# Kernel tuning notes

Hardware: AMD Instinct MI355X
Metric: run time of the kernel (lower is better)

Reference implementation:

```python
import jax, jax.numpy as jnp
import numpy as np

B, T, D, H = 8, 2048, 2048, 128  # batch, seq_len, d_model, head_size
NEG = -1e9


def setup_inputs() -> dict:
    key = jax.random.key(0)
    k0, k1, k2, k3 = jax.random.split(key, 4)
    x = jax.random.normal(k0, (B, T, D), dtype=jnp.float32)
    s = 1.0 / np.sqrt(D)
    Wq = jax.random.normal(k1, (D, H), dtype=jnp.float32) * s
    Wk = jax.random.normal(k2, (D, H), dtype=jnp.float32) * s
    Wv = jax.random.normal(k3, (D, H), dtype=jnp.float32) * s
    return {"x": x, "Wq": Wq, "Wk": Wk, "Wv": Wv}


def reference(x, Wq, Wk, Wv):
    # projections: [B,T,H]
    q = jnp.einsum('btd,dh->bth', x, Wq)
    k = jnp.einsum('btd,dh->bth', x, Wk)
    v = jnp.einsum('btd,dh->bth', x, Wv)
    # NOTE: module multiplies by sqrt(head_size) (faithful to source)
    wei = jnp.einsum('bqh,bkh->bqk', q, k) * jnp.sqrt(jnp.float32(H))
    causal = jnp.tril(jnp.ones((T, T), dtype=bool))
    wei = jnp.where(causal, wei, jnp.float32(NEG))
    wei = jax.nn.softmax(wei, axis=-1)
    # dropout is identity (deterministic=True / rate=0)
    out = jnp.einsum('bqk,bkh->bqh', wei, v)
    return out
```

## Files before the change

kernel.cpp:

```cpp
#include <hip/hip_runtime.h>
#include <math.h>

#define B_ 8
#define T_ 2048
#define D_ 2048
#define H_ 128
#define M_ (B_ * T_)

typedef __bf16 bf16x8 __attribute__((ext_vector_type(8)));
typedef __bf16 bf16x4 __attribute__((ext_vector_type(4)));
typedef float f32x4 __attribute__((ext_vector_type(4)));

#define MFMA(a, b, c) __builtin_amdgcn_mfma_f32_16x16x32_bf16(a, b, c, 0, 0, 0)

#define QH_OFF 0
#define QL_OFF (1 * 2097152)
#define KH_OFF (2 * 2097152)
#define KL_OFF (3 * 2097152)
#define VT_OFF (4 * 2097152)
#define WTH_OFF (5 * 2097152)
#define WTL_OFF (WTH_OFF + 786432)

__global__ __launch_bounds__(256) void prep_kernel(
    const float* __restrict__ Wq, const float* __restrict__ Wk,
    const float* __restrict__ Wv, __bf16* __restrict__ wt_hi,
    __bf16* __restrict__ wt_lo) {
  const int z = blockIdx.y;
  const int k0 = blockIdx.x * 64;
  const float* W = z == 0 ? Wq : z == 1 ? Wk : Wv;
  __shared__ float tile[64][132];
  const int t = threadIdx.x;
#pragma unroll
  for (int it = 0; it < 8; ++it) {
    int f4 = it * 256 + t;
    int row = f4 >> 5, c = (f4 & 31) << 2;
    *(float4*)&tile[row][c] = *(const float4*)&W[(size_t)(k0 + row) * H_ + c];
  }
  __syncthreads();
  int n = t >> 1, kh = (t & 1) << 5;
  __bf16 h[32], l[32];
#pragma unroll
  for (int kk = 0; kk < 32; ++kk) {
    float x = tile[kh + kk][n];
    __bf16 hi = (__bf16)x;
    h[kk] = hi;
    l[kk] = (__bf16)(x - (float)hi);
  }
  size_t base = (size_t)(z * H_ + n) * D_ + k0 + kh;
#pragma unroll
  for (int c = 0; c < 4; ++c) {
    *(bf16x8*)&wt_hi[base + c * 8] = *(bf16x8*)&h[c * 8];
    *(bf16x8*)&wt_lo[base + c * 8] = *(bf16x8*)&l[c * 8];
  }
}

#define WSTR 36
#define XSTR 72

__global__ __launch_bounds__(512, 2) void proj_kernel(
    const float* __restrict__ X, const __bf16* __restrict__ wt_hi,
    const __bf16* __restrict__ wt_lo, __bf16* __restrict__ qh,
    __bf16* __restrict__ ql, __bf16* __restrict__ kh,
    __bf16* __restrict__ kl, __bf16* __restrict__ vt) {
  __shared__ __align__(16) __bf16 Wh[384 * WSTR];
  __shared__ __align__(16) __bf16 Wl[384 * WSTR];
  __shared__ __align__(16) __bf16 Xs[64 * XSTR];
  const int t = threadIdx.x;
  const int wv = t >> 6, lane = t & 63;
  const int l15 = lane & 15, quad = lane >> 4, q8 = quad * 8;
  const int m0 = blockIdx.x * 64;
  const int nb = wv * 48;
  const int xm = t >> 3, xk = (t & 7) << 2;
  const float* xgp = X + (size_t)(m0 + xm) * D_ + xk;
  f32x4 acc[4][3] = {};
  float4 xr = *(const float4*)xgp;
  bf16x8 whr[3], wlr[3];
#pragma unroll
  for (int p = 0; p < 3; ++p) {
    int c = t + (p << 9);
    int n = c >> 2, o = (c & 3) << 3;
    whr[p] = *(const bf16x8*)(wt_hi + (size_t)n * D_ + o);
    wlr[p] = *(const bf16x8*)(wt_lo + (size_t)n * D_ + o);
  }
  for (int ks = 0; ks < 64; ++ks) {
    __syncthreads();
    {
      __bf16 h0 = (__bf16)xr.x, h1 = (__bf16)xr.y, h2 = (__bf16)xr.z,
             h3 = (__bf16)xr.w;
      bf16x4 hv = {h0, h1, h2, h3};
      bf16x4 lv = {(__bf16)(xr.x - (float)h0), (__bf16)(xr.y - (float)h1),
                   (__bf16)(xr.z - (float)h2), (__bf16)(xr.w - (float)h3)};
      *(bf16x4*)&Xs[xm * XSTR + xk] = hv;
      *(bf16x4*)&Xs[xm * XSTR + 32 + xk] = lv;
    }
#pragma unroll
    for (int p = 0; p < 3; ++p) {
      int c = t + (p << 9);
      int n = c >> 2, o = (c & 3) << 3;
      bf16x4 a, b, cc, d;
#pragma unroll
      for (int j = 0; j < 4; ++j) {
        a[j] = whr[p][j];
        b[j] = whr[p][j + 4];
        cc[j] = wlr[p][j];
        d[j] = wlr[p][j + 4];
      }
      *(bf16x4*)&Wh[n * WSTR + o] = a;
      *(bf16x4*)&Wh[n * WSTR + o + 4] = b;
      *(bf16x4*)&Wl[n * WSTR + o] = cc;
      *(bf16x4*)&Wl[n * WSTR + o + 4] = d;
    }
    if (ks < 63) {
      const int ko = (ks + 1) << 5;
      xr = *(const float4*)(xgp + ko);
#pragma unroll
      for (int p = 0; p < 3; ++p) {
        int c = t + (p << 9);
        int n = c >> 2, o = (c & 3) << 3;
        whr[p] = *(const bf16x8*)(wt_hi + (size_t)n * D_ + ko + o);
        wlr[p] = *(const bf16x8*)(wt_lo + (size_t)n * D_ + ko + o);
      }
    }
    __syncthreads();
    bf16x8 ah[4], al[4];
#pragma unroll
    for (int mg = 0; mg < 4; ++mg) {
      ah[mg] = *(bf16x8*)&Xs[(mg * 16 + l15) * XSTR + q8];
      al[mg] = *(bf16x8*)&Xs[(mg * 16 + l15) * XSTR + 32 + q8];
    }
#pragma unroll
    for (int nt = 0; nt < 3; ++nt) {
      const int n = nb + nt * 16 + l15;
      bf16x4 b0 = *(bf16x4*)&Wh[n * WSTR + q8];
      bf16x4 b1 = *(bf16x4*)&Wh[n * WSTR + q8 + 4];
      bf16x4 b2 = *(bf16x4*)&Wl[n * WSTR + q8];
      bf16x4 b3 = *(bf16x4*)&Wl[n * WSTR + q8 + 4];
      bf16x8 bh, bl;
#pragma unroll
      for (int j = 0; j < 4; ++j) {
        bh[j] = b0[j];
        bh[j + 4] = b1[j];
        bl[j] = b2[j];
        bl[j + 4] = b3[j];
      }
#pragma unroll
      for (int mg = 0; mg < 4; ++mg) {
        acc[mg][nt] = MFMA(ah[mg], bh, acc[mg][nt]);
        acc[mg][nt] = MFMA(al[mg], bh, acc[mg][nt]);
        acc[mg][nt] = MFMA(ah[mg], bl, acc[mg][nt]);
      }
    }
  }
#pragma unroll
  for (int nt = 0; nt < 3; ++nt) {
    int ncb = nb + nt * 16;
    int z = ncb >> 7;
    int h = (ncb & 127) + l15;
#pragma unroll
    for (int mg = 0; mg < 4; ++mg) {
      int r0 = m0 + mg * 16 + quad * 4;
      if (z == 2) {
        int b = m0 >> 11;
        int tt0 = (m0 & 2047) + mg * 16 + quad * 4;
        bf16x4 pv = {(__bf16)acc[mg][nt][0], (__bf16)acc[mg][nt][1],
                     (__bf16)acc[mg][nt][2], (__bf16)acc[mg][nt][3]};
        *(bf16x4*)&vt[(size_t)(b * H_ + h) * T_ + tt0] = pv;
      } else {
        __bf16* dh = z == 0 ? qh : kh;
        __bf16* dl = z == 0 ? ql : kl;
#pragma unroll
        for (int reg = 0; reg < 4; ++reg) {
          float v = acc[mg][nt][reg];
          __bf16 hi = (__bf16)v;
          dh[(size_t)(r0 + reg) * H_ + h] = hi;
          dl[(size_t)(r0 + reg) * H_ + h] = (__bf16)(v - (float)hi);
        }
      }
    }
  }
}

__global__ __launch_bounds__(512, 2) void attn_kernel(
    const __bf16* __restrict__ qh, const __bf16* __restrict__ qlo,
    const __bf16* __restrict__ kh, const __bf16* __restrict__ klo,
    const __bf16* __restrict__ vt, float* __restrict__ out) {
  const int t = threadIdx.x;
  const int wv = t >> 6, st = wv >> 2, cw = wv & 3;
  const int lane = t & 63, l15 = lane & 15, quad = lane >> 4;
  const int j = blockIdx.x, b = j >> 5, pi = j & 31;
  const int qlidx = (st == 0) ? pi : 63 - pi;
  const int t0 = qlidx * 32;
  const int nkt = (qlidx >> 1) + 1;
  __shared__ __align__(16) __bf16 Pbuf[8][32 * 72];
  __shared__ __align__(16) float Obuf[2][32 * 132];
  __shared__ float mlb[2][4][32], llb[2][4][32];
  const size_t qrow0 = (size_t)b * T_ + t0;
  bf16x8 qfh[2][4], qfl[2][4];
#pragma unroll
  for (int mg = 0; mg < 2; ++mg)
#pragma unroll
    for (int ds = 0; ds < 4; ++ds) {
      size_t off = (qrow0 + mg * 16 + l15) * H_ + ds * 32 + quad * 8;
      qfh[mg][ds] = *(const bf16x8*)(qh + off);
      qfl[mg][ds] = *(const bf16x8*)(qlo + off);
    }
  f32x4 O[2][8] = {};
  float ms[2][4], ls[2][4];
#pragma unroll
  for (int mg = 0; mg < 2; ++mg)
#pragma unroll
    for (int reg = 0; reg < 4; ++reg) {
      ms[mg][reg] = -INFINITY;
      ls[mg][reg] = 0.f;
    }
  const __bf16* vtb = vt + (size_t)b * H_ * T_;
  const float scale = 11.313708498984761f;
  for (int kt_i = cw; kt_i < nkt; kt_i += 4) {
    const int kt = kt_i * 64;
    f32x4 S[2][4] = {};
#pragma unroll
    for (int ds = 0; ds < 4; ++ds)
#pragma unroll
      for (int ct = 0; ct < 4; ++ct) {
        size_t koff =
            ((size_t)b * T_ + kt + ct * 16 + l15) * H_ + ds * 32 + quad * 8;
        bf16x8 bh = *(const bf16x8*)(kh + koff);
        bf16x8 bl = *(const bf16x8*)(klo + koff);
#pragma unroll
        for (int mg = 0; mg < 2; ++mg) {
          S[mg][ct] = MFMA(qfh[mg][ds], bh, S[mg][ct]);
          S[mg][ct] = MFMA(qfl[mg][ds], bh, S[mg][ct]);
          S[mg][ct] = MFMA(qfh[mg][ds], bl, S[mg][ct]);
        }
      }
    const bool diag = (kt_i == nkt - 1);
#pragma unroll
    for (int mg = 0; mg < 2; ++mg)
#pragma unroll
      for (int ct = 0; ct < 4; ++ct)
#pragma unroll
        for (int reg = 0; reg < 4; ++reg) {
          float s = S[mg][ct][reg] * scale;
          if (diag && (kt + ct * 16 + l15 > t0 + mg * 16 + quad * 4 + reg))
            s = -1e30f;
          S[mg][ct][reg] = s;
        }
    float al_[2][4];
#pragma unroll
    for (int mg = 0; mg < 2; ++mg)
#pragma unroll
      for (int reg = 0; reg < 4; ++reg) {
        float r = fmaxf(fmaxf(S[mg][0][reg], S[mg][1][reg]),
                        fmaxf(S[mg][2][reg], S[mg][3][reg]));
        r = fmaxf(r, __shfl_xor(r, 1));
        r = fmaxf(r, __shfl_xor(r, 2));
        r = fmaxf(r, __shfl_xor(r, 4));
        r = fmaxf(r, __shfl_xor(r, 8));
        float mn = fmaxf(ms[mg][reg], r);
        float a = __expf(ms[mg][reg] - mn);
        ms[mg][reg] = mn;
        float ps = 0.f;
#pragma unroll
        for (int ct = 0; ct < 4; ++ct) {
          float p = __expf(S[mg][ct][reg] - mn);
          S[mg][ct][reg] = p;
          ps += p;
        }
        ps += __shfl_xor(ps, 1);
        ps += __shfl_xor(ps, 2);
        ps += __shfl_xor(ps, 4);
        ps += __shfl_xor(ps, 8);
        ls[mg][reg] = ls[mg][reg] * a + ps;
        al_[mg][reg] = a;
      }
#pragma unroll
    for (int mg = 0; mg < 2; ++mg)
#pragma unroll
      for (int ht = 0; ht < 8; ++ht)
#pragma unroll
        for (int reg = 0; reg < 4; ++reg) O[mg][ht][reg] *= al_[mg][reg];
#pragma unroll
    for (int mg = 0; mg < 2; ++mg)
#pragma unroll
      for (int ct = 0; ct < 4; ++ct)
#pragma unroll
        for (int reg = 0; reg < 4; ++reg)
          Pbuf[wv][(mg * 16 + quad * 4 + reg) * 72 + ct * 16 + l15] =
              (__bf16)S[mg][ct][reg];
#pragma unroll
    for (int ks = 0; ks < 2; ++ks) {
      bf16x8 pf0 = *(bf16x8*)&Pbuf[wv][(l15)*72 + ks * 32 + quad * 8];
      bf16x8 pf1 = *(bf16x8*)&Pbuf[wv][(16 + l15) * 72 + ks * 32 + quad * 8];
#pragma unroll
      for (int ht = 0; ht < 8; ++ht) {
        bf16x8 vf = *(const bf16x8*)&vtb[(size_t)(ht * 16 + l15) * T_ + kt +
                                         ks * 32 + quad * 8];
        O[0][ht] = MFMA(pf0, vf, O[0][ht]);
        O[1][ht] = MFMA(pf1, vf, O[1][ht]);
      }
    }
  }
  if (l15 == 0) {
#pragma unroll
    for (int mg = 0; mg < 2; ++mg)
#pragma unroll
      for (int reg = 0; reg < 4; ++reg) {
        mlb[st][cw][mg * 16 + quad * 4 + reg] = ms[mg][reg];
        llb[st][cw][mg * 16 + quad * 4 + reg] = ls[mg][reg];
      }
  }
  for (int i = t; i < 2 * 32 * 132; i += 512) ((float*)Obuf)[i] = 0.f;
  __syncthreads();
  float aw[2][4];
#pragma unroll
  for (int mg = 0; mg < 2; ++mg)
#pragma unroll
    for (int reg = 0; reg < 4; ++reg) {
      int row = mg * 16 + quad * 4 + reg;
      float M = fmaxf(fmaxf(mlb[st][0][row], mlb[st][1][row]),
                      fmaxf(mlb[st][2][row], mlb[st][3][row]));
      float L = 0.f;
#pragma unroll
      for (int w = 0; w < 4; ++w)
        L += llb[st][w][row] * __expf(mlb[st][w][row] - M);
      aw[mg][reg] = __expf(ms[mg][reg] - M) / L;
    }
#pragma unroll
  for (int mg = 0; mg < 2; ++mg)
#pragma unroll
    for (int ht = 0; ht < 8; ++ht)
#pragma unroll
      for (int reg = 0; reg < 4; ++reg)
        atomicAdd(&Obuf[st][(mg * 16 + quad * 4 + reg) * 132 + ht * 16 + l15],
                  O[mg][ht][reg] * aw[mg][reg]);
  __syncthreads();
  {
    const int stw = t >> 8, tt = t & 255;
    const int qlw = (stw == 0) ? pi : 63 - pi;
    const size_t obase = ((size_t)b * T_ + qlw * 32) * H_;
#pragma unroll
    for (int i = 0; i < 4; ++i) {
      int f4 = i * 256 + tt;
      int row = f4 >> 5, c = (f4 & 31) << 2;
      *(float4*)&out[obase + (size_t)row * H_ + c] =
          *(float4*)&Obuf[stw][row * 132 + c];
    }
  }
}

extern "C" void kernel_launch(void* const* d_in, const int* in_sizes, int n_in,
                              void* d_out, int out_size, void* d_ws, size_t ws_size,
                              hipStream_t stream) {
  const float* x = (const float*)d_in[0];
  const float* Wq = (const float*)d_in[1];
  const float* Wk = (const float*)d_in[2];
  const float* Wv = (const float*)d_in[3];
  __bf16* ws = (__bf16*)d_ws;
  float* out = (float*)d_out;
  prep_kernel<<<dim3(32, 3), 256, 0, stream>>>(Wq, Wk, Wv, ws + WTH_OFF,
                                               ws + WTL_OFF);
  proj_kernel<<<256, 512, 0, stream>>>(x, ws + WTH_OFF, ws + WTL_OFF,
                                       ws + QH_OFF, ws + QL_OFF, ws + KH_OFF,
                                       ws + KL_OFF, ws + VT_OFF);
  attn_kernel<<<256, 512, 0, stream>>>(ws + QH_OFF, ws + QL_OFF, ws + KH_OFF,
                                       ws + KL_OFF, ws + VT_OFF, out);
}
```

Before: 410.0 us.

## Give each attention block one query tile with eight-way key split

Before, each block handled two paired query tiles (early and late) with four waves splitting keys per tile. Now each block processes a single 32-row query tile, all eight waves split its key tiles, and the grid doubles to 512 blocks. Blocks are ordered so early and late tiles interleave and the batch index varies fastest. The intent is finer-grained work distribution for better load balance across CUs. The cost is that short tiles leave most waves idle and the merge step now combines eight partial softmax states.

```diff
diff --git a/kernel.cpp b/kernel.cpp
--- a/kernel.cpp
+++ b/kernel.cpp
@@ -185,15 +185,17 @@
     const __bf16* __restrict__ kh, const __bf16* __restrict__ klo,
     const __bf16* __restrict__ vt, float* __restrict__ out) {
   const int t = threadIdx.x;
-  const int wv = t >> 6, st = wv >> 2, cw = wv & 3;
+  const int wv = t >> 6;
   const int lane = t & 63, l15 = lane & 15, quad = lane >> 4;
-  const int j = blockIdx.x, b = j >> 5, pi = j & 31;
-  const int qlidx = (st == 0) ? pi : 63 - pi;
+  const int j = blockIdx.x;
+  const int b = j & 7;
+  const int p = j >> 3;
+  const int qlidx = (p & 1) ? (63 - (p >> 1)) : (p >> 1);
   const int t0 = qlidx * 32;
   const int nkt = (qlidx >> 1) + 1;
   __shared__ __align__(16) __bf16 Pbuf[8][32 * 72];
-  __shared__ __align__(16) float Obuf[2][32 * 132];
-  __shared__ float mlb[2][4][32], llb[2][4][32];
+  __shared__ __align__(16) float Obuf[32 * 132];
+  __shared__ float mlb[8][32], llb[8][32];
   const size_t qrow0 = (size_t)b * T_ + t0;
   bf16x8 qfh[2][4], qfl[2][4];
 #pragma unroll
@@ -215,7 +217,7 @@
     }
   const __bf16* vtb = vt + (size_t)b * H_ * T_;
   const float scale = 11.313708498984761f;
-  for (int kt_i = cw; kt_i < nkt; kt_i += 4) {
+  for (int kt_i = wv; kt_i < nkt; kt_i += 8) {
     const int kt = kt_i * 64;
     f32x4 S[2][4] = {};
 #pragma unroll
@@ -262,9 +264,9 @@
         float ps = 0.f;
 #pragma unroll
         for (int ct = 0; ct < 4; ++ct) {
-          float p = __expf(S[mg][ct][reg] - mn);
-          S[mg][ct][reg] = p;
-          ps += p;
+          float p_ = __expf(S[mg][ct][reg] - mn);
+          S[mg][ct][reg] = p_;
+          ps += p_;
         }
         ps += __shfl_xor(ps, 1);
         ps += __shfl_xor(ps, 2);
@@ -305,11 +307,12 @@
     for (int mg = 0; mg < 2; ++mg)
 #pragma unroll
       for (int reg = 0; reg < 4; ++reg) {
-        mlb[st][cw][mg * 16 + quad * 4 + reg] = ms[mg][reg];
-        llb[st][cw][mg * 16 + quad * 4 + reg] = ls[mg][reg];
-      }
-  }
-  for (int i = t; i < 2 * 32 * 132; i += 512) ((float*)Obuf)[i] = 0.f;
+        mlb[wv][mg * 16 + quad * 4 + reg] = ms[mg][reg];
+        llb[wv][mg * 16 + quad * 4 + reg] = ls[mg][reg];
+      }
+  }
+  __syncthreads();
+  for (int i = t; i < 32 * 132; i += 512) Obuf[i] = 0.f;
   __syncthreads();
   float aw[2][4];
 #pragma unroll
@@ -317,12 +320,12 @@
 #pragma unroll
     for (int reg = 0; reg < 4; ++reg) {
       int row = mg * 16 + quad * 4 + reg;
-      float M = fmaxf(fmaxf(mlb[st][0][row], mlb[st][1][row]),
-                      fmaxf(mlb[st][2][row], mlb[st][3][row]));
+      float M = mlb[0][row];
+#pragma unroll
+      for (int w = 1; w < 8; ++w) M = fmaxf(M, mlb[w][row]);
       float L = 0.f;
 #pragma unroll
-      for (int w = 0; w < 4; ++w)
-        L += llb[st][w][row] * __expf(mlb[st][w][row] - M);
+      for (int w = 0; w < 8; ++w) L += llb[w][row] * __expf(mlb[w][row] - M);
       aw[mg][reg] = __expf(ms[mg][reg] - M) / L;
     }
 #pragma unroll
@@ -331,19 +334,17 @@
     for (int ht = 0; ht < 8; ++ht)
 #pragma unroll
       for (int reg = 0; reg < 4; ++reg)
-        atomicAdd(&Obuf[st][(mg * 16 + quad * 4 + reg) * 132 + ht * 16 + l15],
+        atomicAdd(&Obuf[(mg * 16 + quad * 4 + reg) * 132 + ht * 16 + l15],
                   O[mg][ht][reg] * aw[mg][reg]);
   __syncthreads();
   {
-    const int stw = t >> 8, tt = t & 255;
-    const int qlw = (stw == 0) ? pi : 63 - pi;
-    const size_t obase = ((size_t)b * T_ + qlw * 32) * H_;
-#pragma unroll
-    for (int i = 0; i < 4; ++i) {
-      int f4 = i * 256 + tt;
+    const size_t obase = ((size_t)b * T_ + t0) * H_;
+#pragma unroll
+    for (int i = 0; i < 2; ++i) {
+      int f4 = i * 512 + t;
       int row = f4 >> 5, c = (f4 & 31) << 2;
       *(float4*)&out[obase + (size_t)row * H_ + c] =
-          *(float4*)&Obuf[stw][row * 132 + c];
+          *(float4*)&Obuf[row * 132 + c];
     }
   }
 }
@@ -362,6 +363,6 @@
   proj_kernel<<<256, 512, 0, stream>>>(x, ws + WTH_OFF, ws + WTL_OFF,
                                        ws + QH_OFF, ws + QL_OFF, ws + KH_OFF,
                                        ws + KL_OFF, ws + VT_OFF);
-  attn_kernel<<<256, 512, 0, stream>>>(ws + QH_OFF, ws + QL_OFF, ws + KH_OFF,
+  attn_kernel<<<512, 512, 0, stream>>>(ws + QH_OFF, ws + QL_OFF, ws + KH_OFF,
                                        ws + KL_OFF, ws + VT_OFF, out);
 }
```

Result: slower. 442.3 us (+7.9%).
